# Performance work log

Hardware: AMD Instinct MI355X
Metric: run time of the kernel (lower is better)

The kernel has to match this reference:

```python
import jax, jax.numpy as jnp
import numpy as np

N_ATOMS = 1_000_000
N_GRAPHS = 8192
FEA_DIM = 64
HIDDEN = 32
N_HEAD = 3


def setup_inputs() -> dict:
    key = jax.random.key(0)
    k1, k2, k3, k4, k5, k6 = jax.random.split(key, 6)
    atom_feas = jax.random.normal(k1, (N_ATOMS, FEA_DIM), dtype=jnp.float32)
    atom_owner = jnp.sort(jax.random.randint(k2, (N_ATOMS,), 0, N_GRAPHS))
    s1 = 1.0 / np.sqrt(FEA_DIM)
    s2 = 1.0 / np.sqrt(HIDDEN)
    W1 = jax.random.uniform(k3, (FEA_DIM, HIDDEN), jnp.float32, -s1, s1)
    b1 = jax.random.uniform(k4, (HIDDEN,), jnp.float32, -s1, s1)
    W2 = jax.random.uniform(k5, (HIDDEN, N_HEAD), jnp.float32, -s2, s2)
    b2 = jax.random.uniform(k6, (N_HEAD,), jnp.float32, -s2, s2)
    return {"atom_feas": atom_feas, "atom_owner": atom_owner,
            "W1": W1, "b1": b1, "W2": W2, "b2": b2}


def reference(atom_feas, atom_owner, W1, b1, W2, b2):
    # key MLP: Linear -> SiLU -> Linear, producing per-atom, per-head logits [N, H]
    h = jax.nn.silu(atom_feas @ W1 + b1)
    logits = h @ W2 + b2  # [N, H]
    # per-graph (segment) softmax over atoms, independently per head
    seg_max = jax.ops.segment_max(logits, atom_owner, num_segments=N_GRAPHS)  # [G, H]
    e = jnp.exp(logits - seg_max[atom_owner])
    denom = jax.ops.segment_sum(e, atom_owner, num_segments=N_GRAPHS)  # [G, H]
    w = e / denom[atom_owner]  # [N, H]
    # attention-weighted pooling: per graph, atom_fea.T @ w -> [D, H] flattened row-major
    outer = (atom_feas[:, :, None] * w[:, None, :]).reshape(atom_feas.shape[0], FEA_DIM * N_HEAD)
    crystal_feas = jax.ops.segment_sum(outer, atom_owner, num_segments=N_GRAPHS)  # [G, D*H]
    return crystal_feas
```

## Files before the change

kernel.cpp:

```cpp
#include <hip/hip_runtime.h>
#include <math.h>
#include <stdint.h>

#define NFEA    64
#define NHEAD   3
#define PSTRIDE 256
#define KSLOT   4

typedef float v2f __attribute__((ext_vector_type(2)));

__global__ void gar_starts(const int* __restrict__ owner, int* __restrict__ starts,
                           int n_atoms, int n_graphs)
{
  int a = blockIdx.x * blockDim.x + threadIdx.x;
  if (a >= n_atoms) return;
  int cur  = owner[a];
  int prev = (a == 0) ? -1 : owner[a - 1];
  for (int g = prev + 1; g <= cur; ++g) starts[g] = a;
  if (a == n_atoms - 1)
    for (int g = cur + 1; g <= n_graphs; ++g) starts[g] = n_atoms;
}

__global__ __launch_bounds__(256, 3) void gar_fused(
    const float* __restrict__ atom_feas,
    const int*   __restrict__ owner,
    const int*   __restrict__ starts,
    const float* __restrict__ W1, const float* __restrict__ b1,
    const float* __restrict__ W2, const float* __restrict__ b2,
    float* __restrict__ partials,
    int n_atoms, int n_graphs)
{
  __shared__ __align__(16) float4 e4[256];
  const int tid = threadIdx.x;
  const int blockstart = blockIdx.x * 256;
  const int a = blockstart + tid;
  const bool act = a < n_atoms;
  const int ar = act ? a : n_atoms - 1;

  const float4* __restrict__ xrow = (const float4*)(atom_feas + (size_t)ar * NFEA);
  float4 xr[16];
#pragma unroll
  for (int q = 0; q < 16; ++q) xr[q] = xrow[q];
  asm volatile("" ::: "memory");

  v2f h[16];
#pragma unroll
  for (int j = 0; j < 16; ++j) h[j] = ((const v2f*)b1)[j];

#pragma unroll
  for (int q = 0; q < 16; ++q) {
    float xs[4] = {xr[q].x, xr[q].y, xr[q].z, xr[q].w};
#pragma unroll
    for (int dd = 0; dd < 4; ++dd) {
      v2f xd2 = {xs[dd], xs[dd]};
      const v2f* wrow = ((const v2f*)W1) + (q * 4 + dd) * 16;
#pragma unroll
      for (int jj = 0; jj < 16; ++jj)
        h[jj] = __builtin_elementwise_fma(xd2, wrow[jj], h[jj]);
    }
  }
  float l0 = b2[0], l1 = b2[1], l2 = b2[2];
#pragma unroll
  for (int jj = 0; jj < 16; ++jj) {
#pragma unroll
    for (int cc = 0; cc < 2; ++cc) {
      float hj = h[jj][cc];
      float s = hj * __builtin_amdgcn_rcpf(1.0f + __expf(-hj));
      int k = 2 * jj + cc;
      l0 = fmaf(s, W2[k * 3 + 0], l0);
      l1 = fmaf(s, W2[k * 3 + 1], l1);
      l2 = fmaf(s, W2[k * 3 + 2], l2);
    }
  }
  e4[tid] = make_float4(act ? __expf(l0) : 0.f,
                        act ? __expf(l1) : 0.f,
                        act ? __expf(l2) : 0.f, 0.f);
  __syncthreads();

  const int blockend = (blockstart + 256 < n_atoms) ? blockstart + 256 : n_atoms;
  const int g0 = owner[blockstart];
  const int g1 = owner[blockend - 1];
  const int w = tid >> 6, t = tid & 63;

  for (int g = g0 + w; g <= g1; g += 4) {
    const int gs0 = starts[g];
    int lo = gs0;           if (lo < blockstart) lo = blockstart;
    int hi = starts[g + 1]; if (hi > blockend)   hi = blockend;
    if (lo >= hi) continue;

    float a0 = 0.f, a1 = 0.f, a2 = 0.f;
    float dd0 = 0.f, dd1 = 0.f, dd2 = 0.f;
    for (int i = lo; i < hi; ++i) {
      float4 ev = e4[i - blockstart];
      float  xv = atom_feas[(size_t)i * NFEA + t];
      a0 = fmaf(ev.x, xv, a0);
      a1 = fmaf(ev.y, xv, a1);
      a2 = fmaf(ev.z, xv, a2);
      dd0 += ev.x; dd1 += ev.y; dd2 += ev.z;
    }
    const int slot = blockIdx.x - (gs0 >> 8);
    if (slot < KSLOT - 1) {
      float* P = partials + ((size_t)slot * n_graphs + g) * PSTRIDE;
      P[t * 3 + 0] = a0; P[t * 3 + 1] = a1; P[t * 3 + 2] = a2;
      if (t == 0) { P[192] = dd0; P[193] = dd1; P[194] = dd2; }
    } else {
      float* P = partials + ((size_t)(KSLOT - 1) * n_graphs + g) * PSTRIDE;
      atomicAdd(P + t * 3 + 0, a0);
      atomicAdd(P + t * 3 + 1, a1);
      atomicAdd(P + t * 3 + 2, a2);
      if (t == 0) { atomicAdd(P + 192, dd0); atomicAdd(P + 193, dd1); atomicAdd(P + 194, dd2); }
    }
  }
}

__global__ __launch_bounds__(256, 8) void gar_reduce(
    const int* __restrict__ starts,
    const float* __restrict__ partials,
    float* __restrict__ out, int n_graphs)
{
  const int g = blockIdx.x * 4 + (threadIdx.x >> 6);
  const int t = threadIdx.x & 63;
  if (g >= n_graphs) return;
  const int s0 = starts[g], s1 = starts[g + 1];

  const float* P3 = partials + ((size_t)(KSLOT - 1) * n_graphs + g) * PSTRIDE;
  float n0 = P3[t * 3 + 0], n1 = P3[t * 3 + 1], n2 = P3[t * 3 + 2];
  float dn0 = P3[192], dn1 = P3[193], dn2 = P3[194];

  int span = 0;
  if (s1 > s0) span = ((s1 - 1) >> 8) - (s0 >> 8) + 1;
  const int kmax = span < (KSLOT - 1) ? span : (KSLOT - 1);
  for (int k = 0; k < kmax; ++k) {
    const float* P = partials + ((size_t)k * n_graphs + g) * PSTRIDE;
    n0 += P[t * 3 + 0]; n1 += P[t * 3 + 1]; n2 += P[t * 3 + 2];
    dn0 += P[192]; dn1 += P[193]; dn2 += P[194];
  }
  float* og = out + (size_t)g * (NFEA * NHEAD);
  og[t * 3 + 0] = dn0 > 0.f ? n0 / dn0 : 0.f;
  og[t * 3 + 1] = dn1 > 0.f ? n1 / dn1 : 0.f;
  og[t * 3 + 2] = dn2 > 0.f ? n2 / dn2 : 0.f;
}

extern "C" void kernel_launch(void* const* d_in, const int* in_sizes, int n_in,
                              void* d_out, int out_size, void* d_ws, size_t ws_size,
                              hipStream_t stream)
{
  const float* atom_feas = (const float*)d_in[0];
  const int*   owner     = (const int*)d_in[1];
  const float* W1        = (const float*)d_in[2];
  const float* b1        = (const float*)d_in[3];
  const float* W2        = (const float*)d_in[4];
  const float* b2        = (const float*)d_in[5];
  float* out = (float*)d_out;

  const int n_atoms  = in_sizes[1];
  const int n_graphs = out_size / (NFEA * NHEAD);

  int* starts = (int*)d_ws;
  const size_t par_off = (((size_t)(n_graphs + 1) * sizeof(int)) + 255) & ~(size_t)255;
  float* partials = (float*)((char*)d_ws + par_off);

  hipMemsetAsync(partials + (size_t)(KSLOT - 1) * n_graphs * PSTRIDE, 0,
                 (size_t)n_graphs * PSTRIDE * sizeof(float), stream);

  hipLaunchKernelGGL(gar_starts, dim3((n_atoms + 255) / 256), dim3(256), 0, stream,
                     owner, starts, n_atoms, n_graphs);
  hipLaunchKernelGGL(gar_fused, dim3((n_atoms + 255) / 256), dim3(256), 0, stream,
                     atom_feas, owner, starts, W1, b1, W2, b2, partials,
                     n_atoms, n_graphs);
  hipLaunchKernelGGL(gar_reduce, dim3((n_graphs + 3) / 4), dim3(256), 0, stream,
                     starts, partials, out, n_graphs);
}
```

Baseline: 484.4 us.

## Split each graph's atom range across all four waves and combine via LDS

Instead of giving whole graphs to waves round-robin, all four waves now walk every graph in the block, each taking every fourth atom. The per-wave partial sums are combined through a shared-memory buffer, and one wave writes or atomically adds the result. This balances load when graphs are uneven within a 256-atom block, at the cost of two block-wide barriers per graph. The compiler fence after the row load also becomes a scheduling barrier.

Measured after the change: 414.1 us. 14.5% less time.

```diff
diff --git a/kernel.cpp b/kernel.cpp
--- a/kernel.cpp
+++ b/kernel.cpp
@@ -31,6 +31,7 @@
     int n_atoms, int n_graphs)
 {
   __shared__ __align__(16) float4 e4[256];
+  __shared__ __align__(16) float4 comb[4][64];
   const int tid = threadIdx.x;
   const int blockstart = blockIdx.x * 256;
   const int a = blockstart + tid;
@@ -41,7 +42,7 @@
   float4 xr[16];
 #pragma unroll
   for (int q = 0; q < 16; ++q) xr[q] = xrow[q];
-  asm volatile("" ::: "memory");
+  __builtin_amdgcn_sched_barrier(0);
 
   v2f h[16];
 #pragma unroll
@@ -82,7 +83,7 @@
   const int g1 = owner[blockend - 1];
   const int w = tid >> 6, t = tid & 63;
 
-  for (int g = g0 + w; g <= g1; g += 4) {
+  for (int g = g0; g <= g1; ++g) {
     const int gs0 = starts[g];
     int lo = gs0;           if (lo < blockstart) lo = blockstart;
     int hi = starts[g + 1]; if (hi > blockend)   hi = blockend;
@@ -90,7 +91,8 @@
 
     float a0 = 0.f, a1 = 0.f, a2 = 0.f;
     float dd0 = 0.f, dd1 = 0.f, dd2 = 0.f;
-    for (int i = lo; i < hi; ++i) {
+#pragma unroll 4
+    for (int i = lo + w; i < hi; i += 4) {
       float4 ev = e4[i - blockstart];
       float  xv = atom_feas[(size_t)i * NFEA + t];
       a0 = fmaf(ev.x, xv, a0);
@@ -98,18 +100,29 @@
       a2 = fmaf(ev.z, xv, a2);
       dd0 += ev.x; dd1 += ev.y; dd2 += ev.z;
     }
-    const int slot = blockIdx.x - (gs0 >> 8);
-    if (slot < KSLOT - 1) {
-      float* P = partials + ((size_t)slot * n_graphs + g) * PSTRIDE;
-      P[t * 3 + 0] = a0; P[t * 3 + 1] = a1; P[t * 3 + 2] = a2;
-      if (t == 0) { P[192] = dd0; P[193] = dd1; P[194] = dd2; }
-    } else {
-      float* P = partials + ((size_t)(KSLOT - 1) * n_graphs + g) * PSTRIDE;
-      atomicAdd(P + t * 3 + 0, a0);
-      atomicAdd(P + t * 3 + 1, a1);
-      atomicAdd(P + t * 3 + 2, a2);
-      if (t == 0) { atomicAdd(P + 192, dd0); atomicAdd(P + 193, dd1); atomicAdd(P + 194, dd2); }
+    const float ddsel = t == 0 ? dd0 : t == 1 ? dd1 : t == 2 ? dd2 : 0.f;
+    comb[w][t] = make_float4(a0, a1, a2, ddsel);
+    __syncthreads();
+    if (w == (g & 3)) {
+      float4 c0 = comb[0][t], c1 = comb[1][t], c2 = comb[2][t], c3 = comb[3][t];
+      float s0 = c0.x + c1.x + c2.x + c3.x;
+      float s1 = c0.y + c1.y + c2.y + c3.y;
+      float s2 = c0.z + c1.z + c2.z + c3.z;
+      float sd = c0.w + c1.w + c2.w + c3.w;
+      const int slot = blockIdx.x - (gs0 >> 8);
+      if (slot < KSLOT - 1) {
+        float* P = partials + ((size_t)slot * n_graphs + g) * PSTRIDE;
+        P[t * 3 + 0] = s0; P[t * 3 + 1] = s1; P[t * 3 + 2] = s2;
+        if (t < 3) P[192 + t] = sd;
+      } else {
+        float* P = partials + ((size_t)(KSLOT - 1) * n_graphs + g) * PSTRIDE;
+        atomicAdd(P + t * 3 + 0, s0);
+        atomicAdd(P + t * 3 + 1, s1);
+        atomicAdd(P + t * 3 + 2, s2);
+        if (t < 3) atomicAdd(P + 192 + t, sd);
+      }
     }
+    __syncthreads();
   }
 }
 
```
